# Optimization experiments

Measured on AMD Instinct MI355X. Metric: run time of the kernel, lower is better.

## Reference

```python
import jax, jax.numpy as jnp
import numpy as np

N = 20000      # nodes per graph
E = 320000     # edges per graph (before self-loops)
G = 256        # graphs (strings) per side
VOCAB = 128    # NUMBER_EMBEDDINGS
D_IN = 128
HID = 64
H = 4
D_OUT = 128
NEG_SLOPE = 0.2  # PyG GATConv leaky_relu slope


def _gat(x, edge_index, W, att_s, att_d, bias, concat):
    """PyG GATConv: gather -> per-edge logits -> segment softmax over dst -> scatter.
    x: [N, F_in], W: [F_in, H*C], att_s/att_d: [H, C], bias: [H*C] or [C].
    Self-loops are added (PyG default add_self_loops=True)."""
    n = x.shape[0]
    h, c = att_s.shape
    loops = jnp.arange(n)
    src = jnp.concatenate([edge_index[0], loops])  # message sources j
    dst = jnp.concatenate([edge_index[1], loops])  # message targets i
    xh = (x @ W).reshape(n, h, c)                  # [N,H,C]
    a_s = jnp.einsum('nhc,hc->nh', xh, att_s)      # [N,H]
    a_d = jnp.einsum('nhc,hc->nh', xh, att_d)
    logits = jax.nn.leaky_relu(a_s[src] + a_d[dst], NEG_SLOPE)  # [E',H]
    m = jax.ops.segment_max(logits, dst, num_segments=n)
    m = jnp.where(jnp.isfinite(m), m, 0.0)
    e = jnp.exp(logits - m[dst])
    z = jax.ops.segment_sum(e, dst, num_segments=n)
    alpha = e / (z[dst] + 1e-16)                   # [E',H]
    msg = xh[src] * alpha[:, :, None]              # [E',H,C]
    out = jax.ops.segment_sum(msg, dst, num_segments=n)  # [N,H,C]
    out = out.reshape(n, h * c) if concat else out.mean(axis=1)
    return out + bias


def _encode(xi, ei, batch, emb, W1, as1, ad1, b1, lw1, lb1,
            W2, as2, ad2, b2, lw2, lb2, W3, as3, ad3, b3, lw3, lb3):
    e = emb[xi]  # [N, D_IN]
    x = jax.nn.relu(_gat(e, ei, W1, as1, ad1, b1, True) + e @ lw1 + lb1)
    x = jax.nn.relu(_gat(x, ei, W2, as2, ad2, b2, True) + x @ lw2 + lb2)
    x = _gat(x, ei, W3, as3, ad3, b3, False) + x @ lw3 + lb3  # [N, D_OUT]
    s = jax.ops.segment_sum(x, batch, num_segments=G)
    cnt = jax.ops.segment_sum(jnp.ones((x.shape[0],), x.dtype), batch, num_segments=G)
    return s / jnp.maximum(cnt, 1.0)[:, None]  # global_mean_pool -> [G, D_OUT]


def setup_inputs() -> dict:
    key = jax.random.key(0)
    ks = jax.random.split(key, 32)
    hc = H * HID  # 256
    def nrm(k, shape, scale=0.05):
        return jax.random.normal(k, shape, dtype=jnp.float32) * scale
    inp = {
        'x_l': jax.random.randint(ks[0], (N,), 0, VOCAB),
        'edge_l': jax.random.randint(ks[1], (2, E), 0, N),
        'batch_l': jnp.sort(jax.random.randint(ks[2], (N,), 0, G)),
        'x_r': jax.random.randint(ks[3], (N,), 0, VOCAB),
        'edge_r': jax.random.randint(ks[4], (2, E), 0, N),
        'batch_r': jnp.sort(jax.random.randint(ks[5], (N,), 0, G)),
        'emb': nrm(ks[6], (VOCAB, D_IN), 1.0),
        'W1': nrm(ks[7], (D_IN, hc)), 'as1': nrm(ks[8], (H, HID)), 'ad1': nrm(ks[9], (H, HID)),
        'b1': jnp.zeros((hc,), jnp.float32), 'lw1': nrm(ks[10], (D_IN, hc)), 'lb1': jnp.zeros((hc,), jnp.float32),
        'W2': nrm(ks[11], (hc, hc)), 'as2': nrm(ks[12], (H, HID)), 'ad2': nrm(ks[13], (H, HID)),
        'b2': jnp.zeros((hc,), jnp.float32), 'lw2': nrm(ks[14], (hc, hc)), 'lb2': jnp.zeros((hc,), jnp.float32),
        'W3': nrm(ks[15], (hc, H * D_OUT)), 'as3': nrm(ks[16], (H, D_OUT)), 'ad3': nrm(ks[17], (H, D_OUT)),
        'b3': jnp.zeros((D_OUT,), jnp.float32), 'lw3': nrm(ks[18], (hc, D_OUT)), 'lb3': jnp.zeros((D_OUT,), jnp.float32),
    }
    return inp


def reference(x_l, edge_l, batch_l, x_r, edge_r, batch_r, emb,
              W1, as1, ad1, b1, lw1, lb1,
              W2, as2, ad2, b2, lw2, lb2,
              W3, as3, ad3, b3, lw3, lb3):
    params = (emb, W1, as1, ad1, b1, lw1, lb1, W2, as2, ad2, b2, lw2, lb2,
              W3, as3, ad3, b3, lw3, lb3)
    out_l = _encode(x_l, edge_l, batch_l, *params)
    out_r = _encode(x_r, edge_r, batch_r, *params)
    return (out_l, out_r)
```

## Files before the change

kernel.cpp:

```cpp
#include <hip/hip_runtime.h>

#define GG 256

typedef __bf16 bf16x8 __attribute__((ext_vector_type(8)));
typedef __bf16 bf16x4 __attribute__((ext_vector_type(4)));
typedef float floatx4 __attribute__((ext_vector_type(4)));
typedef float f32x2 __attribute__((ext_vector_type(2)));

__device__ __forceinline__ float lrelu(float x) { return x > 0.f ? x : 0.2f * x; }

__device__ __forceinline__ int permM(int m) {
    int g = m >> 6, q = m & 63;
    return (g << 6) | ((q & 3) << 4) | (q >> 2);
}

__device__ __forceinline__ void wt1(const float* __restrict__ B, __bf16* __restrict__ Bt,
                                    int K, int M, int idx) {
    int k = idx / M, m = idx - k * M;
    Bt[(size_t)permM(m) * K + k] = (__bf16)B[idx];
}
__device__ __forceinline__ void wattn1(const float* __restrict__ W,
                                       const float* __restrict__ as_,
                                       const float* __restrict__ ad_,
                                       __bf16* __restrict__ dst, int K, int C, int idx) {
    int j = idx / K, k = idx - j * K;
    float v = 0.f;
    if (j < 8) {
        int h = j & 3;
        const float* att = (j < 4) ? as_ : ad_;
        int M = 4 * C;
        for (int c = 0; c < C; c++) v += W[(size_t)k * M + h * C + c] * att[h * C + c];
    }
    dst[(size_t)j * K + k] = (__bf16)v;
}

__global__ void k_wprep(const float* W1, const float* lw1, const float* as1, const float* ad1,
                        const float* W2, const float* lw2, const float* as2, const float* ad2,
                        const float* W3, const float* lw3, const float* as3, const float* ad3,
                        __bf16* B1t, __bf16* B2t, __bf16* B3t) {
    int idx = blockIdx.x * blockDim.x + threadIdx.x;
    if (idx < 32768) { wt1(W1, B1t, 128, 256, idx); return; }
    idx -= 32768;
    if (idx < 32768) { wt1(lw1, B1t + 256 * 128, 128, 256, idx); return; }
    idx -= 32768;
    if (idx < 2048) { wattn1(W1, as1, ad1, B1t + 512 * 128, 128, 64, idx); return; }
    idx -= 2048;
    if (idx < 65536) { wt1(W2, B2t, 256, 256, idx); return; }
    idx -= 65536;
    if (idx < 65536) { wt1(lw2, B2t + 256 * 256, 256, 256, idx); return; }
    idx -= 65536;
    if (idx < 4096) { wattn1(W2, as2, ad2, B2t + 512 * 256, 256, 64, idx); return; }
    idx -= 4096;
    if (idx < 131072) { wt1(W3, B3t, 256, 512, idx); return; }
    idx -= 131072;
    if (idx < 32768) { wt1(lw3, B3t + 512 * 256, 256, 128, idx); return; }
    idx -= 32768;
    if (idx < 4096) { wattn1(W3, as3, ad3, B3t + 640 * 256, 256, 128, idx); return; }
}

template <int K, bool EMB, bool LINBF>
__global__ __launch_bounds__(256) void k_gemm_all(const __bf16* __restrict__ A,
                                                  const int* __restrict__ xl,
                                                  const int* __restrict__ xr,
                                                  const float* __restrict__ emb,
                                                  const __bf16* __restrict__ Bt,
                                                  int n, int n1, int Mx, int Ml,
                                                  unsigned char* __restrict__ x8, int ldx,
                                                  float* __restrict__ linf,
                                                  __bf16* __restrict__ linb, int ldl,
                                                  const float* __restrict__ bias1,
                                                  const float* __restrict__ bias2,
                                                  float* __restrict__ a_s,
                                                  float* __restrict__ a_d) {
    constexpr int KS = K / 32;
    constexpr int LDK = K + 8;
    constexpr int LPR = K / 8;
    constexpr int NCH = 64 * LPR / 256;
    __shared__ __bf16 S[64 * LDK];
    int tid = threadIdx.x;
    int wave = tid >> 6, lane = tid & 63;
    int row0 = blockIdx.x * 64;
#pragma unroll
    for (int c = 0; c < NCH; c++) {
        int i = tid + c * 256;
        int r = i / LPR, ko = (i - r * LPR) * 8;
        int gr = row0 + r;
        bf16x8 v = {};
        if (gr < n) {
            if (EMB) {
                int xi = (gr < n1) ? xl[gr] : xr[gr - n1];
                const float4* src = (const float4*)(emb + ((size_t)xi << 7) + ko);
                float4 q0 = src[0], q1 = src[1];
                v = bf16x8{(__bf16)q0.x, (__bf16)q0.y, (__bf16)q0.z, (__bf16)q0.w,
                           (__bf16)q1.x, (__bf16)q1.y, (__bf16)q1.z, (__bf16)q1.w};
            } else {
                v = *(const bf16x8*)(A + (size_t)gr * K + ko);
            }
        }
        *(bf16x8*)&S[r * LDK + ko] = v;
    }
    __syncthreads();
    int kOff = (lane >> 4) * 8;
    int colBase = lane & 15;
    bf16x8 af[KS];
#pragma unroll
    for (int ks = 0; ks < KS; ks++)
        af[ks] = *(const bf16x8*)&S[(wave * 16 + colBase) * LDK + ks * 32 + kOff];
    int Mtot = Mx + Ml;
    int gr0 = row0 + wave * 16 + ((lane >> 4) << 2);
    int half = (Mtot / 128) * 64;
    int c0beg = blockIdx.y * half;
    int T = half / 64;
    bf16x8 regs[NCH];
#pragma unroll
    for (int c = 0; c < NCH; c++) {
        int i = tid + c * 256;
        int r = i / LPR, ko = (i - r * LPR) * 8;
        regs[c] = *(const bf16x8*)(Bt + (size_t)(c0beg + r) * K + ko);
    }
    for (int t = 0; t < T; t++) {
        __syncthreads();
#pragma unroll
        for (int c = 0; c < NCH; c++) {
            int i = tid + c * 256;
            int r = i / LPR, ko = (i - r * LPR) * 8;
            *(bf16x8*)&S[r * LDK + ko] = regs[c];
        }
        if (t + 1 < T) {
            int c0n = c0beg + (t + 1) * 64;
#pragma unroll
            for (int c = 0; c < NCH; c++) {
                int i = tid + c * 256;
                int r = i / LPR, ko = (i - r * LPR) * 8;
                regs[c] = *(const bf16x8*)(Bt + (size_t)(c0n + r) * K + ko);
            }
        }
        __syncthreads();
        floatx4 acc[4] = {};
#pragma unroll
        for (int ct = 0; ct < 4; ct++) {
#pragma unroll
            for (int ks = 0; ks < KS; ks++) {
                bf16x8 bf = *(const bf16x8*)&S[(ct * 16 + colBase) * LDK + ks * 32 + kOff];
                acc[ct] = __builtin_amdgcn_mfma_f32_16x16x32_bf16(af[ks], bf, acc[ct], 0, 0, 0);
            }
        }
        int c0 = c0beg + t * 64;
        if (c0 < Mx) {
#pragma unroll
            for (int r = 0; r < 4; r++) {
                int gr = gr0 + r;
                if (gr >= n) continue;
                int p = __builtin_amdgcn_cvt_pk_fp8_f32(acc[0][r], acc[1][r], 0, false);
                p = __builtin_amdgcn_cvt_pk_fp8_f32(acc[2][r], acc[3][r], p, true);
                *(unsigned int*)(x8 + (size_t)gr * ldx + c0 + colBase * 4) = (unsigned int)p;
            }
        } else {
            int c2 = c0 + colBase * 4 - Mx;
#pragma unroll
            for (int r = 0; r < 4; r++) {
                int gr = gr0 + r;
                if (gr >= n) continue;
                float v0 = acc[0][r] + bias1[c2 + 0];
                float v1 = acc[1][r] + bias1[c2 + 1];
                float v2 = acc[2][r] + bias1[c2 + 2];
                float v3 = acc[3][r] + bias1[c2 + 3];
                if (bias2) {
                    v0 += bias2[c2 + 0]; v1 += bias2[c2 + 1];
                    v2 += bias2[c2 + 2]; v3 += bias2[c2 + 3];
                }
                if (LINBF) {
                    bf16x4 o = {(__bf16)v0, (__bf16)v1, (__bf16)v2, (__bf16)v3};
                    *(bf16x4*)(linb + (size_t)gr * ldl + c2) = o;
                } else {
                    float4 o = {v0, v1, v2, v3};
                    *(float4*)(linf + (size_t)gr * ldl + c2) = o;
                }
            }
        }
    }
    if (blockIdx.y == 1) {
        floatx4 acc = {};
        const __bf16* bp = Bt + (size_t)(Mtot + colBase) * K + kOff;
#pragma unroll
        for (int ks = 0; ks < KS; ks++) {
            bf16x8 bf = *(const bf16x8*)(bp + ks * 32);
            acc = __builtin_amdgcn_mfma_f32_16x16x32_bf16(af[ks], bf, acc, 0, 0, 0);
        }
        if (colBase < 8) {
            float* dst = (colBase < 4) ? a_s : a_d;
            int h = colBase & 3;
#pragma unroll
            for (int r = 0; r < 4; r++) {
                int gr = gr0 + r;
                if (gr < n) dst[gr * 4 + h] = acc[r];
            }
        }
    }
}

__global__ void k_hist2(const int* __restrict__ el, const int* __restrict__ er,
                        int E, int n, int* __restrict__ deg) {
    int e = blockIdx.x * blockDim.x + threadIdx.x;
    if (e >= 2 * E) return;
    int d = (e < E) ? el[E + e] : er[E + (e - E)] + n;
    atomicAdd(&deg[d], 1);
}

__global__ __launch_bounds__(1024) void k_scan(int* __restrict__ rp, int n) {
    __shared__ int wsum[16];
    __shared__ int s_carry;
    int lane = threadIdx.x & 63, wid = threadIdx.x >> 6;
    if (threadIdx.x == 0) s_carry = 0;
    __syncthreads();
    for (int base = 0; base < n; base += 1024) {
        int i = base + threadIdx.x;
        int v = (i < n) ? rp[i] : 0;
        int inc = v;
#pragma unroll
        for (int off = 1; off < 64; off <<= 1) {
            int t = __shfl_up(inc, off, 64);
            if (lane >= off) inc += t;
        }
        if (lane == 63) wsum[wid] = inc;
        __syncthreads();
        int carry = s_carry;
        __syncthreads();
        if (wid == 0) {
            int wv = (lane < 16) ? wsum[lane] : 0;
            int winc = wv;
#pragma unroll
            for (int off = 1; off < 16; off <<= 1) {
                int t = __shfl_up(winc, off, 64);
                if (lane >= off) winc += t;
            }
            if (lane < 16) wsum[lane] = winc - wv;
            if (lane == 15) s_carry = carry + winc;
        }
        __syncthreads();
        if (i < n) rp[i] = carry + wsum[wid] + (inc - v);
        __syncthreads();
    }
}

__global__ void k_fill2(const int* __restrict__ el, const int* __restrict__ er,
                        int E, int n, int* __restrict__ rp, int* __restrict__ csr) {
    int e = blockIdx.x * blockDim.x + threadIdx.x;
    if (e >= 2 * E) return;
    int d, s;
    if (e < E) { s = el[e]; d = el[E + e]; }
    else       { s = er[e - E] + n; d = er[E + (e - E)] + n; }
    int pos = atomicAdd(&rp[d], 1);
    csr[pos] = s;
}

__device__ __forceinline__ void dec4(unsigned int u, float* f) {
    f32x2 a = __builtin_amdgcn_cvt_pk_f32_fp8(u, false);
    f32x2 b = __builtin_amdgcn_cvt_pk_f32_fp8(u, true);
    f[0] = a[0]; f[1] = a[1]; f[2] = b[0]; f[3] = b[1];
}

__global__ __launch_bounds__(256) void k_agg12(const int* __restrict__ rp,
                                               const int* __restrict__ csr,
                                               const float* __restrict__ a_s,
                                               const float* __restrict__ a_d,
                                               const unsigned char* __restrict__ x8,
                                               const __bf16* __restrict__ lin,
                                               __bf16* __restrict__ out_bf, int n) {
    int wv = (int)((blockIdx.x * blockDim.x + threadIdx.x) >> 6);
    int lane = threadIdx.x & 63;
    int sub = lane >> 5, sl = lane & 31;
    int node = wv * 2 + sub;
    if (node >= n) return;
    int c0 = sl * 8;
    int h = sl >> 3;
    int start = node ? rp[node - 1] : 0;
    int end = rp[node];
    float ad = a_d[node * 4 + h];
    float z = __expf(lrelu(a_s[node * 4 + h] + ad));
    float acc[8];
    {
        uint2 u = *(const uint2*)(x8 + (size_t)node * 256 + c0);
        float f[8];
        dec4(u.x, f); dec4(u.y, f + 4);
#pragma unroll
        for (int j = 0; j < 8; j++) acc[j] = z * f[j];
    }
    uint2 u0 = {}, u1 = {}, u2 = {};
    float A0 = 0.f, A1 = 0.f, A2 = 0.f;
    if (start < end) {
        int s = csr[start];
        u0 = *(const uint2*)(x8 + (size_t)s * 256 + c0);
        A0 = a_s[s * 4 + h];
    }
    if (start + 1 < end) {
        int s = csr[start + 1];
        u1 = *(const uint2*)(x8 + (size_t)s * 256 + c0);
        A1 = a_s[s * 4 + h];
    }
    if (start + 2 < end) {
        int s = csr[start + 2];
        u2 = *(const uint2*)(x8 + (size_t)s * 256 + c0);
        A2 = a_s[s * 4 + h];
    }
    for (int e = start; e < end; e++) {
        uint2 uc = u0;
        float ac = A0;
        u0 = u1; A0 = A1;
        u1 = u2; A1 = A2;
        if (e + 3 < end) {
            int s = csr[e + 3];
            u2 = *(const uint2*)(x8 + (size_t)s * 256 + c0);
            A2 = a_s[s * 4 + h];
        }
        float w = __expf(lrelu(ac + ad));
        z += w;
        float f[8];
        dec4(uc.x, f); dec4(uc.y, f + 4);
#pragma unroll
        for (int q = 0; q < 8; q++) acc[q] += w * f[q];
    }
    float inv = 1.f / (z + 1e-16f);
    bf16x8 l = *(const bf16x8*)(lin + (size_t)node * 256 + c0);
    bf16x8 r;
#pragma unroll
    for (int j = 0; j < 8; j++)
        r[j] = (__bf16)fmaxf(acc[j] * inv + (float)l[j], 0.f);
    *(bf16x8*)(out_bf + (size_t)node * 256 + c0) = r;
}

__global__ __launch_bounds__(256) void k_agg3(const int* __restrict__ rp,
                                              const int* __restrict__ csr,
                                              const float* __restrict__ a_s,
                                              const float* __restrict__ a_d,
                                              const unsigned int* __restrict__ x8,
                                              float* __restrict__ mean, int n) {
    int wv = (int)((blockIdx.x * blockDim.x + threadIdx.x) >> 6);
    int lane = threadIdx.x & 63;
    int sub = lane >> 5, sl = lane & 31;
    int node = wv * 2 + sub;
    if (node >= n) return;
    int h = sl >> 3;
    int start = node ? rp[node - 1] : 0;
    int end = rp[node];
    float ad = a_d[node * 4 + h];
    float z = __expf(lrelu(a_s[node * 4 + h] + ad));
    float acc[16];
    {
        uint4 u = *(const uint4*)(x8 + (size_t)node * 128 + sl * 4);
        float f[16];
        dec4(u.x, f); dec4(u.y, f + 4); dec4(u.z, f + 8); dec4(u.w, f + 12);
#pragma unroll
        for (int j = 0; j < 16; j++) acc[j] = z * f[j];
    }
    uint4 u0 = {}, u1 = {}, u2 = {};
    float A0 = 0.f, A1 = 0.f, A2 = 0.f;
    if (start < end) {
        int s = csr[start];
        u0 = *(const uint4*)(x8 + (size_t)s * 128 + sl * 4);
        A0 = a_s[s * 4 + h];
    }
    if (start + 1 < end) {
        int s = csr[start + 1];
        u1 = *(const uint4*)(x8 + (size_t)s * 128 + sl * 4);
        A1 = a_s[s * 4 + h];
    }
    if (start + 2 < end) {
        int s = csr[start + 2];
        u2 = *(const uint4*)(x8 + (size_t)s * 128 + sl * 4);
        A2 = a_s[s * 4 + h];
    }
    for (int e = start; e < end; e++) {
        uint4 uc = u0;
        float ac = A0;
        u0 = u1; A0 = A1;
        u1 = u2; A1 = A2;
        if (e + 3 < end) {
            int s = csr[e + 3];
            u2 = *(const uint4*)(x8 + (size_t)s * 128 + sl * 4);
            A2 = a_s[s * 4 + h];
        }
        float w = __expf(lrelu(ac + ad));
        z += w;
        float f[16];
        dec4(uc.x, f); dec4(uc.y, f + 4); dec4(uc.z, f + 8); dec4(uc.w, f + 12);
#pragma unroll
        for (int q = 0; q < 16; q++) acc[q] += w * f[q];
    }
    float scale = 0.25f / (z + 1e-16f);
#pragma unroll
    for (int j = 0; j < 16; j++) {
        float v = acc[j] * scale;
        v += __shfl_xor(v, 8, 64);
        v += __shfl_xor(v, 16, 64);
        acc[j] = v;
    }
    if ((sl & 24) == 0) {
        float4* op = (float4*)(mean + (size_t)node * 128 + sl * 16);
#pragma unroll
        for (int q = 0; q < 4; q++) {
            float4 o = {acc[4 * q], acc[4 * q + 1], acc[4 * q + 2], acc[4 * q + 3]};
            op[q] = o;
        }
    }
}

__global__ __launch_bounds__(128) void k_pool(const float* __restrict__ mean,
                                              const float* __restrict__ lin3,
                                              const float* __restrict__ b3,
                                              const int* __restrict__ bl,
                                              const int* __restrict__ br,
                                              int n, float* __restrict__ out) {
    int g = blockIdx.x, c = threadIdx.x;
    const int* b = (g < GG) ? bl : br;
    int tg = (g < GG) ? g : g - GG;
    int off = (g < GG) ? 0 : n;
    int s, e;
    { int lo = 0, hi = n; while (lo < hi) { int m = (lo + hi) >> 1; if (b[m] < tg) lo = m + 1; else hi = m; } s = lo; }
    { int lo = 0, hi = n; while (lo < hi) { int m = (lo + hi) >> 1; if (b[m] < tg + 1) lo = m + 1; else hi = m; } e = lo; }
    s += off; e += off;
    float acc = 0.f;
    for (int i = s; i < e; i++)
        acc += mean[(size_t)i * 128 + c] + lin3[(size_t)i * 128 + c];
    int cnt = e - s;
    out[(size_t)g * 128 + c] = cnt > 0 ? acc / (float)cnt + b3[c] : 0.f;
}

static inline int cdiv(int a, int b) { return (a + b - 1) / b; }

extern "C" void kernel_launch(void* const* d_in, const int* in_sizes, int n_in,
                              void* d_out, int out_size, void* d_ws, size_t ws_size,
                              hipStream_t stream) {
    const int* x_l = (const int*)d_in[0];
    const int* edge_l = (const int*)d_in[1];
    const int* batch_l = (const int*)d_in[2];
    const int* x_r = (const int*)d_in[3];
    const int* edge_r = (const int*)d_in[4];
    const int* batch_r = (const int*)d_in[5];
    const float* emb = (const float*)d_in[6];
    const float* W1 = (const float*)d_in[7];
    const float* as1 = (const float*)d_in[8];
    const float* ad1 = (const float*)d_in[9];
    const float* b1 = (const float*)d_in[10];
    const float* lw1 = (const float*)d_in[11];
    const float* lb1 = (const float*)d_in[12];
    const float* W2 = (const float*)d_in[13];
    const float* as2 = (const float*)d_in[14];
    const float* ad2 = (const float*)d_in[15];
    const float* b2 = (const float*)d_in[16];
    const float* lw2 = (const float*)d_in[17];
    const float* lb2 = (const float*)d_in[18];
    const float* W3 = (const float*)d_in[19];
    const float* as3 = (const float*)d_in[20];
    const float* ad3 = (const float*)d_in[21];
    const float* b3 = (const float*)d_in[22];
    const float* lw3 = (const float*)d_in[23];
    const float* lb3 = (const float*)d_in[24];

    const int n = in_sizes[0];
    const int E = in_sizes[1] / 2;
    const int N2 = 2 * n;

    float* MEAN = (float*)d_ws;
    float* L3 = MEAN + (size_t)N2 * 128;
    float* a_s = L3 + (size_t)N2 * 128;
    float* a_d = a_s + (size_t)N2 * 4;
    int* rp = (int*)(a_d + (size_t)N2 * 4);
    int* csr = rp + N2;
    __bf16* LINb = (__bf16*)(csr + 2 * E);
    unsigned char* X8a = (unsigned char*)(LINb + (size_t)N2 * 256);
    unsigned char* X8b = X8a + (size_t)N2 * 256;
    __bf16* Abf = (__bf16*)(X8b + (size_t)N2 * 512);
    __bf16* B1t = Abf + (size_t)N2 * 256;
    __bf16* B2t = B1t + 528 * 128;
    __bf16* B3t = B2t + 528 * 256;

    const int TB = 256;
    dim3 blk(TB);

    k_wprep<<<cdiv(370688, TB), blk, 0, stream>>>(W1, lw1, as1, ad1, W2, lw2, as2, ad2,
                                                  W3, lw3, as3, ad3, B1t, B2t, B3t);

    hipMemsetAsync(rp, 0, sizeof(int) * (size_t)N2, stream);
    k_hist2<<<cdiv(2 * E, TB), blk, 0, stream>>>(edge_l, edge_r, E, n, rp);
    k_scan<<<1, 1024, 0, stream>>>(rp, N2);
    k_fill2<<<cdiv(2 * E, TB), blk, 0, stream>>>(edge_l, edge_r, E, n, rp, csr);

    k_gemm_all<128, true, true><<<dim3(cdiv(N2, 64), 2), blk, 0, stream>>>(
        nullptr, x_l, x_r, emb, B1t, N2, n, 256, 256, X8a, 256, nullptr, LINb, 256, lb1, b1, a_s, a_d);
    k_agg12<<<cdiv(N2, 8), blk, 0, stream>>>(rp, csr, a_s, a_d, X8a, LINb, Abf, N2);

    k_gemm_all<256, false, true><<<dim3(cdiv(N2, 64), 2), blk, 0, stream>>>(
        Abf, nullptr, nullptr, nullptr, B2t, N2, n, 256, 256, X8a, 256, nullptr, LINb, 256, lb2, b2, a_s, a_d);
    k_agg12<<<cdiv(N2, 8), blk, 0, stream>>>(rp, csr, a_s, a_d, X8a, LINb, Abf, N2);

    k_gemm_all<256, false, false><<<dim3(cdiv(N2, 64), 2), blk, 0, stream>>>(
        Abf, nullptr, nullptr, nullptr, B3t, N2, n, 512, 128, X8b, 512, L3, nullptr, 128, lb3, nullptr, a_s, a_d);
    k_agg3<<<cdiv(N2, 8), blk, 0, stream>>>(rp, csr, a_s, a_d, (const unsigned int*)X8b, MEAN, N2);
    k_pool<<<2 * GG, 128, 0, stream>>>(MEAN, L3, b3, batch_l, batch_r, n, (float*)d_out);
}
```

Before: 484.3 us.

## Replace single-block prefix scan with three-phase multi-block scan

The CSR row-pointer exclusive scan ran in one 1024-thread block that looped serially over all chunks of the degree array. It is now split into a per-block scan that writes block totals, a single-wave scan of those totals, and a pass that adds the block offsets. This spreads the scan across many CUs but adds two extra kernel launches and a small partials buffer, which holds at most 64 blocks.

```diff
diff --git a/kernel.cpp b/kernel.cpp
--- a/kernel.cpp
+++ b/kernel.cpp
@@ -207,40 +207,51 @@
     atomicAdd(&deg[d], 1);
 }
 
-__global__ __launch_bounds__(1024) void k_scan(int* __restrict__ rp, int n) {
+__global__ __launch_bounds__(1024) void k_scan1(int* __restrict__ rp, int n,
+                                                int* __restrict__ part) {
     __shared__ int wsum[16];
-    __shared__ int s_carry;
+    int i = blockIdx.x * 1024 + threadIdx.x;
     int lane = threadIdx.x & 63, wid = threadIdx.x >> 6;
-    if (threadIdx.x == 0) s_carry = 0;
+    int v = (i < n) ? rp[i] : 0;
+    int inc = v;
+#pragma unroll
+    for (int off = 1; off < 64; off <<= 1) {
+        int t = __shfl_up(inc, off, 64);
+        if (lane >= off) inc += t;
+    }
+    if (lane == 63) wsum[wid] = inc;
     __syncthreads();
-    for (int base = 0; base < n; base += 1024) {
-        int i = base + threadIdx.x;
-        int v = (i < n) ? rp[i] : 0;
-        int inc = v;
-#pragma unroll
-        for (int off = 1; off < 64; off <<= 1) {
-            int t = __shfl_up(inc, off, 64);
-            if (lane >= off) inc += t;
-        }
-        if (lane == 63) wsum[wid] = inc;
-        __syncthreads();
-        int carry = s_carry;
-        __syncthreads();
-        if (wid == 0) {
-            int wv = (lane < 16) ? wsum[lane] : 0;
-            int winc = wv;
-#pragma unroll
-            for (int off = 1; off < 16; off <<= 1) {
-                int t = __shfl_up(winc, off, 64);
-                if (lane >= off) winc += t;
-            }
-            if (lane < 16) wsum[lane] = winc - wv;
-            if (lane == 15) s_carry = carry + winc;
-        }
-        __syncthreads();
-        if (i < n) rp[i] = carry + wsum[wid] + (inc - v);
-        __syncthreads();
-    }
+    if (wid == 0) {
+        int wv = (lane < 16) ? wsum[lane] : 0;
+        int winc = wv;
+#pragma unroll
+        for (int off = 1; off < 16; off <<= 1) {
+            int t = __shfl_up(winc, off, 64);
+            if (lane >= off) winc += t;
+        }
+        if (lane < 16) wsum[lane] = winc - wv;
+        if (lane == 15) part[blockIdx.x] = winc;
+    }
+    __syncthreads();
+    if (i < n) rp[i] = wsum[wid] + (inc - v);
+}
+
+__global__ void k_scan2(int* __restrict__ part, int nb) {
+    int lane = threadIdx.x;
+    int v = (lane < nb) ? part[lane] : 0;
+    int inc = v;
+#pragma unroll
+    for (int off = 1; off < 64; off <<= 1) {
+        int t = __shfl_up(inc, off, 64);
+        if (lane >= off) inc += t;
+    }
+    if (lane < nb) part[lane] = inc - v;
+}
+
+__global__ __launch_bounds__(1024) void k_scan3(int* __restrict__ rp, int n,
+                                                const int* __restrict__ part) {
+    int i = blockIdx.x * 1024 + threadIdx.x;
+    if (i < n) rp[i] += part[blockIdx.x];
 }
 
 __global__ void k_fill2(const int* __restrict__ el, const int* __restrict__ er,
@@ -460,6 +471,7 @@
     const int n = in_sizes[0];
     const int E = in_sizes[1] / 2;
     const int N2 = 2 * n;
+    const int NB = cdiv(N2, 1024);
 
     float* MEAN = (float*)d_ws;
     float* L3 = MEAN + (size_t)N2 * 128;
@@ -467,7 +479,8 @@
     float* a_d = a_s + (size_t)N2 * 4;
     int* rp = (int*)(a_d + (size_t)N2 * 4);
     int* csr = rp + N2;
-    __bf16* LINb = (__bf16*)(csr + 2 * E);
+    int* part = csr + 2 * E;
+    __bf16* LINb = (__bf16*)(part + 64);
     unsigned char* X8a = (unsigned char*)(LINb + (size_t)N2 * 256);
     unsigned char* X8b = X8a + (size_t)N2 * 256;
     __bf16* Abf = (__bf16*)(X8b + (size_t)N2 * 512);
@@ -483,7 +496,9 @@
 
     hipMemsetAsync(rp, 0, sizeof(int) * (size_t)N2, stream);
     k_hist2<<<cdiv(2 * E, TB), blk, 0, stream>>>(edge_l, edge_r, E, n, rp);
-    k_scan<<<1, 1024, 0, stream>>>(rp, N2);
+    k_scan1<<<NB, 1024, 0, stream>>>(rp, N2, part);
+    k_scan2<<<1, 64, 0, stream>>>(part, NB);
+    k_scan3<<<NB, 1024, 0, stream>>>(rp, N2, part);
     k_fill2<<<cdiv(2 * E, TB), blk, 0, stream>>>(edge_l, edge_r, E, n, rp, csr);
 
     k_gemm_all<128, true, true><<<dim3(cdiv(N2, 64), 2), blk, 0, stream>>>(
```

Result: faster. 446.4 us (-7.8%).
